# Kernel tuning notes

Hardware: AMD Instinct MI355X
Metric: run time of the kernel (lower is better)

Reference implementation:

```python
import jax, jax.numpy as jnp
import numpy as np

N_HEAD = 16  # head_dim = C // N_HEAD = 128


def setup_inputs() -> dict:
    key = jax.random.key(0)
    k1, k2, k3 = jax.random.split(key, 3)
    B, T, C = 2, 2048, 2048
    x = jax.random.normal(k1, (B, T, C), dtype=jnp.float32)
    # c_attn: Linear(C, 3*C), no bias; stored as (in, out) for x @ W
    w_attn = jax.random.normal(k2, (C, 3 * C), dtype=jnp.float32) * (1.0 / np.sqrt(C))
    # c_proj: Linear(C, C), no bias
    w_proj = jax.random.normal(k3, (C, C), dtype=jnp.float32) * (1.0 / np.sqrt(C))
    return {"x": x, "w_attn": w_attn, "w_proj": w_proj}


def reference(x, w_attn, w_proj):
    B, T, C = x.shape
    H = N_HEAD
    D = C // H  # head dimension
    qkv = x @ w_attn                      # [B, T, 3C]
    q, k, v = jnp.split(qkv, 3, axis=-1)  # each [B, T, C]
    # [B, T, C] -> [B, H, T, D]
    q = q.reshape(B, T, H, D).transpose(0, 2, 1, 3)
    k = k.reshape(B, T, H, D).transpose(0, 2, 1, 3)
    v = v.reshape(B, T, H, D).transpose(0, 2, 1, 3)
    scale = 1.0 / np.sqrt(D).astype(np.float32)
    att = jnp.einsum('bhqd,bhkd->bhqk', q, k) * scale  # [B, H, T, T]
    causal = jnp.tril(jnp.ones((T, T), dtype=bool))
    att = jnp.where(causal[None, None, :, :], att, jnp.float32(-jnp.inf))
    att = jax.nn.softmax(att, axis=-1)
    y = jnp.einsum('bhqk,bhkd->bhqd', att, v)  # [B, H, T, D]
    y = y.transpose(0, 2, 1, 3).reshape(B, T, C)
    # all_reduce is identity with number_of_workers=1; dropout=0 (eval)
    return y @ w_proj
```

## Files before the change

kernel.cpp:

```cpp
#include <hip/hip_runtime.h>
#include <hip/hip_bf16.h>
#include <stdint.h>

#define TLEN 2048
#define CDIM 2048
#define BDIM 2
#define HDIM 16
#define DHEAD 128
#define QROW ((size_t)(3 * CDIM))

typedef __bf16 bf16x8 __attribute__((ext_vector_type(8)));
typedef float f32x4 __attribute__((ext_vector_type(4)));

__device__ __forceinline__ uint16_t f32_to_bf16(float f) {
    uint32_t u = __builtin_bit_cast(uint32_t, f);
    uint32_t r = (u + 0x7FFFu + ((u >> 16) & 1u)) >> 16;
    return (uint16_t)r;
}
__device__ __forceinline__ float bf16_to_f32(uint32_t h) {
    uint32_t u = h << 16;
    return __builtin_bit_cast(float, u);
}

__device__ __forceinline__ void gload_lds16(const uint16_t* g, uint16_t* l) {
    __builtin_amdgcn_global_load_lds(
        (const __attribute__((address_space(1))) uint32_t*)g,
        (__attribute__((address_space(3))) uint32_t*)l, 16, 0, 0);
}

__global__ void cvt_f32_bf16(const float* __restrict__ in, uint16_t* __restrict__ out, int n) {
    int i = (blockIdx.x * blockDim.x + threadIdx.x) * 4;
    if (i + 3 < n) {
        float4 f = *reinterpret_cast<const float4*>(in + i);
        ushort4 o;
        o.x = f32_to_bf16(f.x);
        o.y = f32_to_bf16(f.y);
        o.z = f32_to_bf16(f.z);
        o.w = f32_to_bf16(f.w);
        *reinterpret_cast<ushort4*>(out + i) = o;
    }
}

__global__ __launch_bounds__(256) void transpose_cvt(const float* __restrict__ in,
                                                     uint16_t* __restrict__ out,
                                                     int R, int Cc) {
    __shared__ uint16_t tile[64][65];
    int c0 = blockIdx.x * 64;
    int r0 = blockIdx.y * 64;
    int tc = threadIdx.x & 63;
    int t4 = threadIdx.x >> 6;
    for (int rr = t4; rr < 64; rr += 4) {
        tile[rr][tc] = f32_to_bf16(in[(size_t)(r0 + rr) * Cc + c0 + tc]);
    }
    __syncthreads();
    int wr = threadIdx.x & 63;
    for (int cc = t4; cc < 64; cc += 4) {
        out[(size_t)(c0 + cc) * R + r0 + wr] = tile[wr][cc];
    }
}

__global__ __launch_bounds__(256) void transpose_v(const uint16_t* __restrict__ qkv,
                                                   uint16_t* __restrict__ vtg) {
    __shared__ uint16_t tile[64][65];
    int t0 = blockIdx.x * 64;
    int d0 = blockIdx.y * 64;
    int bh = blockIdx.z;
    int b = bh >> 4, h = bh & 15;
    int tc = threadIdx.x & 63;
    int t4 = threadIdx.x >> 6;
    const uint16_t* src = qkv + (size_t)(b * TLEN + t0) * QROW + 2 * CDIM + h * DHEAD + d0;
    for (int rr = t4; rr < 64; rr += 4)
        tile[rr][tc] = src[(size_t)rr * QROW + tc];
    __syncthreads();
    uint16_t* dst = vtg + ((size_t)bh * DHEAD + d0) * TLEN + t0;
    int wr = threadIdx.x & 63;
    for (int cc = t4; cc < 64; cc += 4)
        dst[(size_t)cc * TLEN + wr] = tile[wr][cc];
}

template <int OUT_BF16>
__global__ __launch_bounds__(256) void gemm_bf16_128(const uint16_t* __restrict__ A,
                                                     const uint16_t* __restrict__ Bt,
                                                     void* __restrict__ Cp,
                                                     int M, int N, int K) {
    __shared__ __align__(16) uint16_t As[128 * 32];
    __shared__ __align__(16) uint16_t Bs[128 * 32];
    const int tid = threadIdx.x;
    const int wave = tid >> 6;
    const int lane = tid & 63;
    const int l15 = lane & 15;
    const int quad = lane >> 4;
    const int m0 = blockIdx.y * 128;
    const int n0 = blockIdx.x * 128;
    const int wm = (wave >> 1) * 64;
    const int wn = (wave & 1) * 64;

    f32x4 acc[4][4] = {};

    const int s0 = wave * 2;
    const int lrow = lane >> 2;
    const int lcol = (lane & 3) * 8;
    const uint16_t* Ag = A + (size_t)(m0 + s0 * 16 + lrow) * K + lcol;
    const uint16_t* Bg = Bt + (size_t)(n0 + s0 * 16 + lrow) * K + lcol;
    uint16_t* AsW0 = As + s0 * 512;
    uint16_t* AsW1 = As + (s0 + 1) * 512;
    uint16_t* BsW0 = Bs + s0 * 512;
    uint16_t* BsW1 = Bs + (s0 + 1) * 512;
    const size_t rowStep = (size_t)16 * K;

    for (int k0 = 0; k0 < K; k0 += 32) {
        gload_lds16(Ag + k0, AsW0);
        gload_lds16(Ag + rowStep + k0, AsW1);
        gload_lds16(Bg + k0, BsW0);
        gload_lds16(Bg + rowStep + k0, BsW1);
        __syncthreads();

        bf16x8 af[4], bfr[4];
#pragma unroll
        for (int mi = 0; mi < 4; mi++)
            af[mi] = *reinterpret_cast<const bf16x8*>(
                As + (wm + mi * 16 + l15) * 32 + quad * 8);
#pragma unroll
        for (int ni = 0; ni < 4; ni++)
            bfr[ni] = *reinterpret_cast<const bf16x8*>(
                Bs + (wn + ni * 16 + l15) * 32 + quad * 8);
#pragma unroll
        for (int mi = 0; mi < 4; mi++)
#pragma unroll
            for (int ni = 0; ni < 4; ni++)
                acc[mi][ni] = __builtin_amdgcn_mfma_f32_16x16x32_bf16(
                    af[mi], bfr[ni], acc[mi][ni], 0, 0, 0);
        __syncthreads();
    }

#pragma unroll
    for (int mi = 0; mi < 4; mi++)
#pragma unroll
        for (int ni = 0; ni < 4; ni++)
#pragma unroll
            for (int r = 0; r < 4; r++) {
                int row = m0 + wm + mi * 16 + quad * 4 + r;
                int col = n0 + wn + ni * 16 + l15;
                float v = acc[mi][ni][r];
                if (OUT_BF16)
                    ((uint16_t*)Cp)[(size_t)row * N + col] = f32_to_bf16(v);
                else
                    ((float*)Cp)[(size_t)row * N + col] = v;
            }
}

#define ATT_C1 0.12751743f
#define ATT_C2 17.3123405f

__global__ __launch_bounds__(256) void attn_mfma3(const uint16_t* __restrict__ qkv,
                                                  const uint16_t* __restrict__ vtg,
                                                  uint16_t* __restrict__ y) {
    __shared__ __align__(16) uint16_t Ks[64 * 128];
    __shared__ __align__(16) uint16_t Vts[128 * 64];
    __shared__ __align__(16) uint16_t Ps[4][32 * 72];

    const int tid = threadIdx.x;
    const int wave = tid >> 6;
    const int lane = tid & 63;
    const int l15 = lane & 15;
    const int quad = lane >> 4;
    const int h = blockIdx.y;
    const int b = blockIdx.z;
    const int qblk = (int)gridDim.x - 1 - (int)blockIdx.x;
    const int qbase = qblk * 128 + wave * 32;
    const int kmax = qbase + 31;

    const uint16_t* kg = qkv + (size_t)b * TLEN * QROW + CDIM + h * DHEAD;
    const uint16_t* vg = vtg + (size_t)(b * HDIM + h) * DHEAD * TLEN;
    uint16_t* PsW = Ps[wave];

    int koff[4], voff[4];
#pragma unroll
    for (int i = 0; i < 4; i++) {
        int Lb = (wave * 4 + i) * 64 + lane;
        int key = Lb >> 4;
        int ck = (Lb & 15) ^ (key & 15);
        koff[i] = key * (int)QROW + ck * 8;
        int d = Lb >> 3;
        int cv = (Lb & 7) ^ (d & 7);
        voff[i] = d * TLEN + cv * 8;
    }

    bf16x8 qfrag[2][4];
#pragma unroll
    for (int m = 0; m < 2; m++) {
        const uint16_t* qp =
            qkv + (size_t)(b * TLEN + qbase + m * 16 + l15) * QROW + h * DHEAD + quad * 8;
#pragma unroll
        for (int kc = 0; kc < 4; kc++)
            qfrag[m][kc] = *reinterpret_cast<const bf16x8*>(qp + kc * 32);
    }

    f32x4 oacc[2][8] = {};
    float psum[2] = {0.f, 0.f};

    const int diagT = qblk * 2 + (wave >> 1);
    const int ntiles = qblk * 2 + 2;

    for (int t = 0; t < ntiles; t++) {
        const int j0 = t * 64;
        if (t > 0) __syncthreads();
        {
            const uint16_t* kj = kg + (size_t)j0 * QROW;
            const uint16_t* vj = vg + j0;
#pragma unroll
            for (int i = 0; i < 4; i++) {
                gload_lds16(kj + koff[i], Ks + (wave * 4 + i) * 512);
                gload_lds16(vj + voff[i], Vts + (wave * 4 + i) * 512);
            }
        }
        __syncthreads();
        if (t > diagT) continue;

        const bool masked = (t == diagT);
        const int n0max = masked ? ((kmax - j0) >> 4) : 3;

        f32x4 st[4][2];
#pragma unroll
        for (int n0 = 0; n0 < 4; n0++) {
            if (masked && n0 > n0max) continue;
            bf16x8 kf[4];
#pragma unroll
            for (int kc = 0; kc < 4; kc++) {
                int cpr = (kc * 4 + quad) ^ l15;
                kf[kc] = *reinterpret_cast<const bf16x8*>(
                    Ks + (n0 * 16 + l15) * 128 + cpr * 8);
            }
#pragma unroll
            for (int m = 0; m < 2; m++) {
                f32x4 acc = {};
#pragma unroll
                for (int kc = 0; kc < 4; kc++)
                    acc = __builtin_amdgcn_mfma_f32_16x16x32_bf16(
                        kf[kc], qfrag[m][kc], acc, 0, 0, 0);
                st[n0][m] = acc;
            }
        }

#pragma unroll
        for (int n0 = 0; n0 < 4; n0++) {
            if (masked && n0 > n0max) continue;
#pragma unroll
            for (int m = 0; m < 2; m++) {
                uint32_t pk0, pk1;
                float ps = 0.f;
                float pv[4];
#pragma unroll
                for (int r = 0; r < 4; r++) {
                    float p = exp2f(st[n0][m][r] * ATT_C1 - ATT_C2);
                    if (masked) {
                        int key = j0 + n0 * 16 + quad * 4 + r;
                        int q = qbase + m * 16 + l15;
                        if (key > q) p = 0.f;
                    }
                    uint32_t pb = f32_to_bf16(p);
                    pv[r] = bf16_to_f32(pb);
                    if (r == 0) pk0 = pb;
                    else if (r == 1) pk0 |= pb << 16;
                    else if (r == 2) pk1 = pb;
                    else pk1 |= pb << 16;
                }
                ps = (pv[0] + pv[1]) + (pv[2] + pv[3]);
                psum[m] += ps;
                *reinterpret_cast<uint2*>(PsW + (m * 16 + l15) * 72 + n0 * 16 + quad * 4) =
                    make_uint2(pk0, pk1);
            }
        }

        const int kcend = masked ? (((kmax - j0) >> 5) + 1) : 2;
#pragma unroll
        for (int kc = 0; kc < 2; kc++) {
            if (kc >= kcend) continue;
            bf16x8 pf[2];
#pragma unroll
            for (int m = 0; m < 2; m++)
                pf[m] = *reinterpret_cast<const bf16x8*>(
                    PsW + (m * 16 + l15) * 72 + kc * 32 + quad * 8);
#pragma unroll
            for (int n0 = 0; n0 < 8; n0++) {
                int cpr = (kc * 4 + quad) ^ (l15 & 7);
                bf16x8 vf = *reinterpret_cast<const bf16x8*>(
                    Vts + (n0 * 16 + l15) * 64 + cpr * 8);
#pragma unroll
                for (int m = 0; m < 2; m++)
                    oacc[m][n0] = __builtin_amdgcn_mfma_f32_16x16x32_bf16(
                        pf[m], vf, oacc[m][n0], 0, 0, 0);
            }
        }
    }

#pragma unroll
    for (int m = 0; m < 2; m++) {
        float s = psum[m];
        s += __shfl_xor(s, 16);
        s += __shfl_xor(s, 32);
        psum[m] = 1.0f / s;
    }
    uint16_t* ybase = y + (size_t)(b * TLEN + qbase) * CDIM + h * DHEAD;
#pragma unroll
    for (int m = 0; m < 2; m++)
#pragma unroll
        for (int r = 0; r < 4; r++) {
            float inv = __shfl(psum[m], quad * 4 + r);
#pragma unroll
            for (int n0 = 0; n0 < 8; n0++)
                ybase[(size_t)(m * 16 + quad * 4 + r) * CDIM + n0 * 16 + l15] =
                    f32_to_bf16(oacc[m][n0][r] * inv);
        }
}

extern "C" void kernel_launch(void* const* d_in, const int* in_sizes, int n_in,
                              void* d_out, int out_size, void* d_ws, size_t ws_size,
                              hipStream_t stream) {
    const float* x = (const float*)d_in[0];
    const float* w_attn = (const float*)d_in[1];
    const float* w_proj = (const float*)d_in[2];
    float* out = (float*)d_out;

    const int M = BDIM * TLEN;
    const int K = CDIM;
    const int N3 = 3 * CDIM;

    char* ws = (char*)d_ws;
    uint16_t* xb = (uint16_t*)(ws);
    uint16_t* waT = (uint16_t*)(ws + 16777216);
    uint16_t* wpT = (uint16_t*)(ws + 41943040);
    uint16_t* qkvb = (uint16_t*)(ws + 50331648);
    uint16_t* yb = (uint16_t*)(ws + 100663296);
    uint16_t* vtb = xb;

    cvt_f32_bf16<<<(M * K / 4 + 255) / 256, 256, 0, stream>>>(x, xb, M * K);
    transpose_cvt<<<dim3(N3 / 64, K / 64), 256, 0, stream>>>(w_attn, waT, K, N3);
    transpose_cvt<<<dim3(K / 64, K / 64), 256, 0, stream>>>(w_proj, wpT, K, K);
    gemm_bf16_128<1><<<dim3(N3 / 128, M / 128), 256, 0, stream>>>(xb, waT, (void*)qkvb, M, N3, K);
    transpose_v<<<dim3(TLEN / 64, DHEAD / 64, BDIM * HDIM), 256, 0, stream>>>(qkvb, vtb);
    attn_mfma3<<<dim3(TLEN / 128, HDIM, BDIM), 256, 0, stream>>>(qkvb, vtb, yb);
    gemm_bf16_128<0><<<dim3(K / 128, M / 128), 256, 0, stream>>>(yb, wpT, (void*)out, M, K, K);
}
```

Baseline: 452.0 us.

## Fuse V transpose into QKV GEMM epilogue and swizzle GEMM LDS layout

The QKV GEMM now writes the V third of its output directly in transposed per-head layout, removing the separate transpose_v kernel and its extra global read and write pass. It also applies an XOR swizzle to the column block used for LDS staging and fragment reads, aimed at reducing LDS bank conflicts. The transposed V stores are 8-byte writes strided by TLEN, so they are less coalesced than row-major stores. The change to the attention sum is a cosmetic cleanup.

```diff
diff --git a/kernel.cpp b/kernel.cpp
--- a/kernel.cpp
+++ b/kernel.cpp
@@ -59,29 +59,11 @@
     }
 }
 
-__global__ __launch_bounds__(256) void transpose_v(const uint16_t* __restrict__ qkv,
-                                                   uint16_t* __restrict__ vtg) {
-    __shared__ uint16_t tile[64][65];
-    int t0 = blockIdx.x * 64;
-    int d0 = blockIdx.y * 64;
-    int bh = blockIdx.z;
-    int b = bh >> 4, h = bh & 15;
-    int tc = threadIdx.x & 63;
-    int t4 = threadIdx.x >> 6;
-    const uint16_t* src = qkv + (size_t)(b * TLEN + t0) * QROW + 2 * CDIM + h * DHEAD + d0;
-    for (int rr = t4; rr < 64; rr += 4)
-        tile[rr][tc] = src[(size_t)rr * QROW + tc];
-    __syncthreads();
-    uint16_t* dst = vtg + ((size_t)bh * DHEAD + d0) * TLEN + t0;
-    int wr = threadIdx.x & 63;
-    for (int cc = t4; cc < 64; cc += 4)
-        dst[(size_t)cc * TLEN + wr] = tile[wr][cc];
-}
-
-template <int OUT_BF16>
+template <int MODE>
 __global__ __launch_bounds__(256) void gemm_bf16_128(const uint16_t* __restrict__ A,
                                                      const uint16_t* __restrict__ Bt,
                                                      void* __restrict__ Cp,
+                                                     uint16_t* __restrict__ vt,
                                                      int M, int N, int K) {
     __shared__ __align__(16) uint16_t As[128 * 32];
     __shared__ __align__(16) uint16_t Bs[128 * 32];
@@ -99,14 +81,18 @@
 
     const int s0 = wave * 2;
     const int lrow = lane >> 2;
-    const int lcol = (lane & 3) * 8;
-    const uint16_t* Ag = A + (size_t)(m0 + s0 * 16 + lrow) * K + lcol;
-    const uint16_t* Bg = Bt + (size_t)(n0 + s0 * 16 + lrow) * K + lcol;
+    const int swzW = (lrow ^ (lrow >> 2)) & 3;
+    const int cblk = (lane & 3) ^ swzW;
+    const uint16_t* Ag = A + (size_t)(m0 + s0 * 16 + lrow) * K + cblk * 8;
+    const uint16_t* Bg = Bt + (size_t)(n0 + s0 * 16 + lrow) * K + cblk * 8;
     uint16_t* AsW0 = As + s0 * 512;
     uint16_t* AsW1 = As + (s0 + 1) * 512;
     uint16_t* BsW0 = Bs + s0 * 512;
     uint16_t* BsW1 = Bs + (s0 + 1) * 512;
     const size_t rowStep = (size_t)16 * K;
+
+    const int swzR = (l15 ^ (l15 >> 2)) & 3;
+    const int rdblk = (quad ^ swzR) * 8;
 
     for (int k0 = 0; k0 < K; k0 += 32) {
         gload_lds16(Ag + k0, AsW0);
@@ -119,11 +105,11 @@
 #pragma unroll
         for (int mi = 0; mi < 4; mi++)
             af[mi] = *reinterpret_cast<const bf16x8*>(
-                As + (wm + mi * 16 + l15) * 32 + quad * 8);
+                As + (wm + mi * 16 + l15) * 32 + rdblk);
 #pragma unroll
         for (int ni = 0; ni < 4; ni++)
             bfr[ni] = *reinterpret_cast<const bf16x8*>(
-                Bs + (wn + ni * 16 + l15) * 32 + quad * 8);
+                Bs + (wn + ni * 16 + l15) * 32 + rdblk);
 #pragma unroll
         for (int mi = 0; mi < 4; mi++)
 #pragma unroll
@@ -133,20 +119,37 @@
         __syncthreads();
     }
 
+    const bool vmode = (MODE == 2) && (n0 >= 2 * CDIM);
 #pragma unroll
     for (int mi = 0; mi < 4; mi++)
 #pragma unroll
-        for (int ni = 0; ni < 4; ni++)
-#pragma unroll
-            for (int r = 0; r < 4; r++) {
-                int row = m0 + wm + mi * 16 + quad * 4 + r;
+        for (int ni = 0; ni < 4; ni++) {
+            if (vmode) {
                 int col = n0 + wn + ni * 16 + l15;
-                float v = acc[mi][ni][r];
-                if (OUT_BF16)
-                    ((uint16_t*)Cp)[(size_t)row * N + col] = f32_to_bf16(v);
-                else
-                    ((float*)Cp)[(size_t)row * N + col] = v;
-            }
+                int vcol = col - 2 * CDIM;
+                int hh = vcol >> 7, d = vcol & 127;
+                int rowm = m0 + wm + mi * 16 + quad * 4;
+                int bb = rowm >> 11, t = rowm & 2047;
+                uint32_t lo = (uint32_t)f32_to_bf16(acc[mi][ni][0]) |
+                              ((uint32_t)f32_to_bf16(acc[mi][ni][1]) << 16);
+                uint32_t hi = (uint32_t)f32_to_bf16(acc[mi][ni][2]) |
+                              ((uint32_t)f32_to_bf16(acc[mi][ni][3]) << 16);
+                *reinterpret_cast<uint2*>(
+                    vt + ((size_t)((bb * HDIM + hh) * DHEAD + d)) * TLEN + t) =
+                    make_uint2(lo, hi);
+            } else {
+#pragma unroll
+                for (int r = 0; r < 4; r++) {
+                    int row = m0 + wm + mi * 16 + quad * 4 + r;
+                    int col = n0 + wn + ni * 16 + l15;
+                    float v = acc[mi][ni][r];
+                    if (MODE != 0)
+                        ((uint16_t*)Cp)[(size_t)row * N + col] = f32_to_bf16(v);
+                    else
+                        ((float*)Cp)[(size_t)row * N + col] = v;
+                }
+            }
+        }
 }
 
 #define ATT_C1 0.12751743f
@@ -248,7 +251,6 @@
 #pragma unroll
             for (int m = 0; m < 2; m++) {
                 uint32_t pk0, pk1;
-                float ps = 0.f;
                 float pv[4];
 #pragma unroll
                 for (int r = 0; r < 4; r++) {
@@ -265,8 +267,7 @@
                     else if (r == 2) pk1 = pb;
                     else pk1 |= pb << 16;
                 }
-                ps = (pv[0] + pv[1]) + (pv[2] + pv[3]);
-                psum[m] += ps;
+                psum[m] += (pv[0] + pv[1]) + (pv[2] + pv[3]);
                 *reinterpret_cast<uint2*>(PsW + (m * 16 + l15) * 72 + n0 * 16 + quad * 4) =
                     make_uint2(pk0, pk1);
             }
@@ -337,8 +338,7 @@
     cvt_f32_bf16<<<(M * K / 4 + 255) / 256, 256, 0, stream>>>(x, xb, M * K);
     transpose_cvt<<<dim3(N3 / 64, K / 64), 256, 0, stream>>>(w_attn, waT, K, N3);
     transpose_cvt<<<dim3(K / 64, K / 64), 256, 0, stream>>>(w_proj, wpT, K, K);
-    gemm_bf16_128<1><<<dim3(N3 / 128, M / 128), 256, 0, stream>>>(xb, waT, (void*)qkvb, M, N3, K);
-    transpose_v<<<dim3(TLEN / 64, DHEAD / 64, BDIM * HDIM), 256, 0, stream>>>(qkvb, vtb);
+    gemm_bf16_128<2><<<dim3(N3 / 128, M / 128), 256, 0, stream>>>(xb, waT, (void*)qkvb, vtb, M, N3, K);
     attn_mfma3<<<dim3(TLEN / 128, HDIM, BDIM), 256, 0, stream>>>(qkvb, vtb, yb);
-    gemm_bf16_128<0><<<dim3(K / 128, M / 128), 256, 0, stream>>>(yb, wpT, (void*)out, M, K, K);
-}
+    gemm_bf16_128<0><<<dim3(K / 128, M / 128), 256, 0, stream>>>(yb, wpT, (void*)out, nullptr, M, K, K);
+}
```

Measured after the change: 448.1 us. About the same (-0.9%).
